# Optimization experiments

Hardware: AMD Instinct MI355X
Metric: run time of the kernel (lower is better)

## Reference

```python
import jax, jax.numpy as jnp
import numpy as np

B, T, IN, H = 64, 512, 128, 512


def _lstm_layer(x, W_ih, W_hh, b_ih, b_hh):
    """Single unidirectional LSTM layer, batch_first input x: [B,T,in].
    PyTorch gate order: i, f, g, o. Returns outputs [B,T,H]."""
    # Precompute input contribution for all timesteps: [T,B,4H]
    xg = jnp.einsum('bti,gi->tbg', x, W_ih) + (b_ih + b_hh)
    Bt = x.shape[0]
    h0 = jnp.zeros((Bt, W_hh.shape[1]), x.dtype)
    c0 = jnp.zeros_like(h0)

    def step(carry, xt):
        h, c = carry
        g = xt + h @ W_hh.T  # [B,4H]
        i, f, gg, o = jnp.split(g, 4, axis=-1)
        i = jax.nn.sigmoid(i)
        f = jax.nn.sigmoid(f)
        gg = jnp.tanh(gg)
        o = jax.nn.sigmoid(o)
        c = f * c + i * gg
        h = o * jnp.tanh(c)
        return (h, c), h

    (_, _), hs = jax.lax.scan(step, (h0, c0), xg)
    return jnp.transpose(hs, (1, 0, 2))  # [B,T,H]


def setup_inputs() -> dict:
    key = jax.random.key(0)
    ks = jax.random.split(key, 11)
    s_in = 1.0 / np.sqrt(H)  # PyTorch LSTM init scale U(-1/sqrt(H), 1/sqrt(H))
    u = lambda k, shape: jax.random.uniform(k, shape, jnp.float32, -s_in, s_in)
    return {
        'x': jax.random.normal(ks[0], (B, T, IN), jnp.float32),
        'W_ih0': u(ks[1], (4 * H, IN)),
        'W_hh0': u(ks[2], (4 * H, H)),
        'b_ih0': u(ks[3], (4 * H,)),
        'b_hh0': u(ks[4], (4 * H,)),
        'W_ih1': u(ks[5], (4 * H, H)),
        'W_hh1': u(ks[6], (4 * H, H)),
        'b_ih1': u(ks[7], (4 * H,)),
        'b_hh1': u(ks[8], (4 * H,)),
        'W_fc': u(ks[9], (1, H)),
        'b_fc': u(ks[10], (1,)),
    }


def reference(x, W_ih0, W_hh0, b_ih0, b_hh0, W_ih1, W_hh1, b_ih1, b_hh1, W_fc, b_fc):
    out = _lstm_layer(x, W_ih0, W_hh0, b_ih0, b_hh0)
    out = _lstm_layer(out, W_ih1, W_hh1, b_ih1, b_hh1)
    logits = out[:, -1, :] @ W_fc.T + b_fc  # [B,1]
    return logits
```

## Files before the change

kernel.cpp:

```cpp
#include <hip/hip_runtime.h>


#define NWG 64
#define NB 64
#define NT 512
#define NH 512
#define FPAD 16

typedef float f32x4 __attribute__((ext_vector_type(4)));
typedef __bf16 bf16x4 __attribute__((ext_vector_type(4)));
typedef __bf16 bf16x8 __attribute__((ext_vector_type(8)));

__device__ __forceinline__ bf16x4 ld8_bypass(const __bf16* p) {
    unsigned long long v = __hip_atomic_load((const unsigned long long*)p,
                                             __ATOMIC_RELAXED, __HIP_MEMORY_SCOPE_AGENT);
    bf16x4 r; __builtin_memcpy(&r, &v, 8); return r;
}

__device__ __forceinline__ void st8_bypass(__bf16* p, unsigned long long v) {
    __hip_atomic_store((unsigned long long*)p, v, __ATOMIC_RELAXED, __HIP_MEMORY_SCOPE_AGENT);
}

__device__ __forceinline__ void wait_flags(const unsigned* flags, unsigned target, int lane) {
    int guard = 0;
    for (;;) {
        unsigned f = __hip_atomic_load((unsigned*)&flags[lane * FPAD],
                                       __ATOMIC_RELAXED, __HIP_MEMORY_SCOPE_AGENT);
        if (__all((int)(f >= target))) break;
        if (++guard > (1 << 17)) break;
    }
}

__global__ void prep_kernel(unsigned short* hs0, unsigned short* hs1, unsigned* flags) {
    int i = blockIdx.x * blockDim.x + threadIdx.x;
    if (i < 2 * NWG * NB * 8) { hs0[i] = 0; hs1[i] = 0; }
    if (i < 2 * NWG * FPAD) flags[i] = 0;
}

template<int KIH, int IS_L0>
__device__ __forceinline__ void layer_body(
    char* Wl, float (*gbuf)[36], float (*c_lds)[8], unsigned short (*hstage)[8],
    int wg,
    const float* __restrict__ W_ih, const float* __restrict__ W_hh,
    const float* __restrict__ b_ih, const float* __restrict__ b_hh,
    const float* __restrict__ x_f32,
    const __bf16* __restrict__ h_in_all,
    __bf16* __restrict__ h_out_all,
    __bf16* __restrict__ hbuf,
    float* __restrict__ h_final,
    unsigned* __restrict__ flags_self,
    const unsigned* __restrict__ flags_dep)
{
    constexpr int KTOT = KIH + NH;
    constexpr int NCH_A = KIH / 32;
    constexpr int NCH_B = NH / 32;
    constexpr int ROWB = KTOT * 2;
    constexpr int BLK = NB * 8;

    const int tid = threadIdx.x;
    const int hcol0 = wg * 8;

    {
        constexpr int CPR = KTOT / 8;
        for (int cid = tid; cid < 32 * CPR; cid += 512) {
            const int r = cid / CPR;
            const int k0 = (cid - r * CPR) * 8;
            const int grow = (r >> 3) * NH + hcol0 + (r & 7);
            const float* src = (k0 < KIH) ? (W_ih + (size_t)grow * KIH + k0)
                                          : (W_hh + (size_t)grow * NH + (k0 - KIH));
            union { __bf16 h[8]; uint4 u; } tmp;
            #pragma unroll
            for (int j = 0; j < 8; ++j) tmp.h[j] = (__bf16)src[j];
            const unsigned off = (unsigned)(r * ROWB) +
                (((unsigned)(2 * k0)) ^ ((unsigned)((r & 7) << 4)));
            *(uint4*)(Wl + off) = tmp.u;
        }
    }

    const int eb = tid >> 3, ec = tid & 7;
    const int hcE = hcol0 + ec;
    const float bI = b_ih[hcE]          + b_hh[hcE];
    const float bF = b_ih[NH + hcE]     + b_hh[NH + hcE];
    const float bG = b_ih[2 * NH + hcE] + b_hh[2 * NH + hcE];
    const float bO = b_ih[3 * NH + hcE] + b_hh[3 * NH + hcE];
    c_lds[eb][ec] = 0.0f;
    __syncthreads();

    const int lane = tid & 63;
    const int wid = tid >> 6;
    const int bt = (wid & 3) * 16;
    const int gt = (wid >> 2) * 16;
    const int arow = bt + (lane & 15);
    const int q4 = ((lane >> 4) & 3) * 4;
    const int brow = gt + (lane & 15);
    const char* wrow = Wl + brow * ROWB;
    const unsigned bsz = (unsigned)((brow & 7) << 4);

    const int aoff = arow * 8 + (q4 & 4);
    const int bsub = (q4 >> 3);

    auto wfrag = [&](int k0) -> bf16x8 {
        const bf16x4 blo = *(const bf16x4*)(wrow + (((unsigned)(2 * (k0 + q4))) ^ bsz));
        const bf16x4 bhi = *(const bf16x4*)(wrow + (((unsigned)(2 * (k0 + 16 + q4))) ^ bsz));
        return __builtin_shufflevector(blo, bhi, 0, 1, 2, 3, 4, 5, 6, 7);
    };

    for (int t = 0; t < NT; ++t) {
        const __bf16* __restrict__ hprev = hbuf + (size_t)(t & 1) * NWG * BLK;
        __bf16* __restrict__ hout = hbuf + (size_t)((t + 1) & 1) * NWG * BLK;

        f32x4 accA0 = {0.f,0.f,0.f,0.f}, accA1 = {0.f,0.f,0.f,0.f};
        f32x4 accB0 = {0.f,0.f,0.f,0.f}, accB1 = {0.f,0.f,0.f,0.f};

        if constexpr (IS_L0 != 0) {
            const float* xb = x_f32 + ((size_t)arow * NT + t) * KIH;
            bf16x8 av[NCH_A];
            #pragma unroll
            for (int kk = 0; kk < NCH_A; ++kk) {
                const float4 lo = *(const float4*)(xb + kk * 32 + q4);
                const float4 hi = *(const float4*)(xb + kk * 32 + 16 + q4);
                const bf16x4 alo = {(__bf16)lo.x, (__bf16)lo.y, (__bf16)lo.z, (__bf16)lo.w};
                const bf16x4 ahi = {(__bf16)hi.x, (__bf16)hi.y, (__bf16)hi.z, (__bf16)hi.w};
                av[kk] = __builtin_shufflevector(alo, ahi, 0, 1, 2, 3, 4, 5, 6, 7);
            }
            #pragma unroll
            for (int kk = 0; kk < NCH_A; ++kk) {
                f32x4& a = (kk & 1) ? accA1 : accA0;
                a = __builtin_amdgcn_mfma_f32_16x16x32_bf16(av[kk], wfrag(kk * 32), a, 0, 0, 0);
            }
            if (t > 0 && wid == 0) wait_flags(flags_self, (unsigned)t, lane);
            __syncthreads();
        } else {
            if (wid == 0) wait_flags(flags_dep, (unsigned)(t + 1), lane);
            if (wid == 1 && t > 0) wait_flags(flags_self, (unsigned)t, lane);
            __syncthreads();
        }

        bf16x4 aBlo[NCH_B], aBhi[NCH_B];
        #pragma unroll
        for (int kk = 0; kk < NCH_B; ++kk) {
            const __bf16* base = hprev + (4 * kk + bsub) * BLK + aoff;
            aBlo[kk] = ld8_bypass(base);
            aBhi[kk] = ld8_bypass(base + 2 * BLK);
        }
        if constexpr (IS_L0 == 0) {
            const __bf16* hA = h_in_all + (size_t)t * NWG * BLK;
            bf16x4 aAlo[NCH_A], aAhi[NCH_A];
            #pragma unroll
            for (int kk = 0; kk < NCH_A; ++kk) {
                const __bf16* base = hA + (4 * kk + bsub) * BLK + aoff;
                aAlo[kk] = ld8_bypass(base);
                aAhi[kk] = ld8_bypass(base + 2 * BLK);
            }
            #pragma unroll
            for (int kk = 0; kk < NCH_A; ++kk) {
                f32x4& a = (kk & 1) ? accA1 : accA0;
                const bf16x8 av = __builtin_shufflevector(aAlo[kk], aAhi[kk], 0,1,2,3,4,5,6,7);
                a = __builtin_amdgcn_mfma_f32_16x16x32_bf16(av, wfrag(kk * 32), a, 0, 0, 0);
            }
        }
        #pragma unroll
        for (int kk = 0; kk < NCH_B; ++kk) {
            f32x4& a = (kk & 1) ? accB1 : accB0;
            const bf16x8 av = __builtin_shufflevector(aBlo[kk], aBhi[kk], 0,1,2,3,4,5,6,7);
            a = __builtin_amdgcn_mfma_f32_16x16x32_bf16(av, wfrag(KIH + kk * 32), a, 0, 0, 0);
        }

        const f32x4 acc = (accA0 + accA1) + (accB0 + accB1);

        #pragma unroll
        for (int i = 0; i < 4; ++i)
            gbuf[bt + ((lane >> 4) & 3) * 4 + i][gt + (lane & 15)] = acc[i];
        __syncthreads();

        {
            const float gi = gbuf[eb][ec]      + bI;
            const float gf = gbuf[eb][8 + ec]  + bF;
            const float gg = gbuf[eb][16 + ec] + bG;
            const float go = gbuf[eb][24 + ec] + bO;
            const float ii = 1.0f / (1.0f + __expf(-gi));
            const float ff = 1.0f / (1.0f + __expf(-gf));
            const float g2 = 2.0f / (1.0f + __expf(-2.0f * gg)) - 1.0f;
            const float oo = 1.0f / (1.0f + __expf(-go));
            const float cn = ff * c_lds[eb][ec] + ii * g2;
            const float th = 2.0f / (1.0f + __expf(-2.0f * cn)) - 1.0f;
            const float hn = oo * th;
            c_lds[eb][ec] = cn;
            const __bf16 hb = (__bf16)hn;
            unsigned short ub;
            __builtin_memcpy(&ub, &hb, 2);
            hstage[eb][ec] = ub;
            if constexpr (IS_L0 == 0) {
                if (t == NT - 1) h_final[(size_t)eb * NH + hcol0 + ec] = hn;
            }
        }
        __syncthreads();

        if (tid < 128) {
            unsigned long long v;
            __builtin_memcpy(&v, &hstage[tid >> 1][(tid & 1) * 4], 8);
            st8_bypass(hout + (size_t)wg * BLK + tid * 4, v);
            if constexpr (IS_L0 != 0)
                st8_bypass(h_out_all + ((size_t)t * NWG + wg) * BLK + tid * 4, v);
        }
        asm volatile("s_waitcnt vmcnt(0)" ::: "memory");
        __syncthreads();
        if (tid == 0)
            __hip_atomic_store(&flags_self[wg * FPAD], (unsigned)(t + 1),
                               __ATOMIC_RELAXED, __HIP_MEMORY_SCOPE_AGENT);
    }
}

__launch_bounds__(512, 2)
__global__ void lstm_fused_kernel(
    const float* W_ih0, const float* W_hh0, const float* b_ih0, const float* b_hh0,
    const float* W_ih1, const float* W_hh1, const float* b_ih1, const float* b_hh1,
    const float* x, __bf16* h0_all, __bf16* hs0, __bf16* hs1,
    float* hfin, unsigned* flags0, unsigned* flags1)
{
    __shared__ __align__(16) char Wl[32 * 2048];
    __shared__ float gbuf[64][36];
    __shared__ float c_lds[64][8];
    __shared__ unsigned short hstage[64][8];

    if (blockIdx.x < NWG) {
        layer_body<128, 1>(Wl, gbuf, c_lds, hstage, blockIdx.x,
                           W_ih0, W_hh0, b_ih0, b_hh0,
                           x, nullptr, h0_all, hs0, nullptr, flags0, nullptr);
    } else {
        layer_body<512, 0>(Wl, gbuf, c_lds, hstage, blockIdx.x - NWG,
                           W_ih1, W_hh1, b_ih1, b_hh1,
                           nullptr, h0_all, nullptr, hs1, hfin, flags1, flags0);
    }
}

__global__ void fc_kernel(const float* __restrict__ hfin,
                          const float* __restrict__ w_fc,
                          const float* __restrict__ b_fc,
                          float* __restrict__ out) {
    __shared__ float red[64][9];
    const int tid = threadIdx.x;
    const int b = tid >> 3, p = tid & 7;
    const int k0 = p * 64;
    float s = 0.f;
    #pragma unroll 8
    for (int k = 0; k < 64; ++k) s += hfin[(size_t)b * NH + k0 + k] * w_fc[k0 + k];
    red[b][p] = s;
    __syncthreads();
    if (p == 0) {
        float a = 0.f;
        #pragma unroll
        for (int j = 0; j < 8; ++j) a += red[b][j];
        out[b] = a + b_fc[0];
    }
}

extern "C" void kernel_launch(void* const* d_in, const int* in_sizes, int n_in,
                              void* d_out, int out_size, void* d_ws, size_t ws_size,
                              hipStream_t stream) {
    const float* x     = (const float*)d_in[0];
    const float* W_ih0 = (const float*)d_in[1];
    const float* W_hh0 = (const float*)d_in[2];
    const float* b_ih0 = (const float*)d_in[3];
    const float* b_hh0 = (const float*)d_in[4];
    const float* W_ih1 = (const float*)d_in[5];
    const float* W_hh1 = (const float*)d_in[6];
    const float* b_ih1 = (const float*)d_in[7];
    const float* b_hh1 = (const float*)d_in[8];
    const float* W_fc  = (const float*)d_in[9];
    const float* b_fc  = (const float*)d_in[10];

    char* ws = (char*)d_ws;
    __bf16*  h0_all = (__bf16*)(ws);
    __bf16*  hs0    = (__bf16*)(ws + 33554432);
    __bf16*  hs1    = (__bf16*)(ws + 33554432 + 131072);
    float*   hfin   = (float*) (ws + 33554432 + 262144);
    unsigned* flags0 = (unsigned*)(ws + 33554432 + 393216);
    unsigned* flags1 = flags0 + NWG * FPAD;

    prep_kernel<<<dim3(256), dim3(256), 0, stream>>>(
        (unsigned short*)hs0, (unsigned short*)hs1, flags0);

    lstm_fused_kernel<<<dim3(2 * NWG), dim3(512), 0, stream>>>(
        W_ih0, W_hh0, b_ih0, b_hh0, W_ih1, W_hh1, b_ih1, b_hh1,
        x, h0_all, hs0, hs1, hfin, flags0, flags1);

    fc_kernel<<<dim3(1), dim3(512), 0, stream>>>(hfin, W_fc, b_fc, (float*)d_out);
}
```

Baseline: 3.117 ms.

## Replace per-workgroup step flags with per-timestep arrival counters and drop ping-pong buffer

The cross-workgroup handshake changes from 64 padded per-workgroup flags to per-timestep counters split into 8 sub-counters. Each workgroup atomically increments one sub-counter, and waiters poll only 8 addresses instead of 64 separate cache lines. Layer 0 now reads its previous hidden state straight from the full h_out_all history, so the duplicate store into a ping-pong buffer is removed. The trade-off is atomic fetch_add contention (8 writers per sub-counter) and counter arrays sized by the number of timesteps.

```diff
diff --git a/kernel.cpp b/kernel.cpp
--- a/kernel.cpp
+++ b/kernel.cpp
@@ -5,7 +5,6 @@
 #define NB 64
 #define NT 512
 #define NH 512
-#define FPAD 16
 
 typedef float f32x4 __attribute__((ext_vector_type(4)));
 typedef __bf16 bf16x4 __attribute__((ext_vector_type(4)));
@@ -21,20 +20,22 @@
     __hip_atomic_store((unsigned long long*)p, v, __ATOMIC_RELAXED, __HIP_MEMORY_SCOPE_AGENT);
 }
 
-__device__ __forceinline__ void wait_flags(const unsigned* flags, unsigned target, int lane) {
+__device__ __forceinline__ void wait_cnt(const unsigned* cnt, int t, int lane) {
+    const unsigned* p = cnt + t * 16 + (lane & 7);
     int guard = 0;
     for (;;) {
-        unsigned f = __hip_atomic_load((unsigned*)&flags[lane * FPAD],
-                                       __ATOMIC_RELAXED, __HIP_MEMORY_SCOPE_AGENT);
-        if (__all((int)(f >= target))) break;
+        unsigned f = __hip_atomic_load((unsigned*)p, __ATOMIC_RELAXED,
+                                       __HIP_MEMORY_SCOPE_AGENT);
+        if (__all((int)(f >= 8u))) break;
         if (++guard > (1 << 17)) break;
     }
 }
 
-__global__ void prep_kernel(unsigned short* hs0, unsigned short* hs1, unsigned* flags) {
+__global__ void prep_kernel(unsigned short* hinit, unsigned short* hs1, unsigned* cnts) {
     int i = blockIdx.x * blockDim.x + threadIdx.x;
-    if (i < 2 * NWG * NB * 8) { hs0[i] = 0; hs1[i] = 0; }
-    if (i < 2 * NWG * FPAD) flags[i] = 0;
+    if (i < NWG * NB * 8) hinit[i] = 0;
+    if (i < 2 * NWG * NB * 8) hs1[i] = 0;
+    if (i < 2 * NT * 16) cnts[i] = 0;
 }
 
 template<int KIH, int IS_L0>
@@ -46,10 +47,11 @@
     const float* __restrict__ x_f32,
     const __bf16* __restrict__ h_in_all,
     __bf16* __restrict__ h_out_all,
+    const __bf16* __restrict__ hinit,
     __bf16* __restrict__ hbuf,
     float* __restrict__ h_final,
-    unsigned* __restrict__ flags_self,
-    const unsigned* __restrict__ flags_dep)
+    unsigned* __restrict__ cnt_self,
+    const unsigned* __restrict__ cnt_dep)
 {
     constexpr int KTOT = KIH + NH;
     constexpr int NCH_A = KIH / 32;
@@ -106,8 +108,15 @@
     };
 
     for (int t = 0; t < NT; ++t) {
-        const __bf16* __restrict__ hprev = hbuf + (size_t)(t & 1) * NWG * BLK;
-        __bf16* __restrict__ hout = hbuf + (size_t)((t + 1) & 1) * NWG * BLK;
+        const __bf16* __restrict__ hprev;
+        __bf16* __restrict__ hout;
+        if constexpr (IS_L0 != 0) {
+            hprev = (t == 0) ? hinit : (h_out_all + (size_t)(t - 1) * NWG * BLK);
+            hout = h_out_all + (size_t)t * NWG * BLK;
+        } else {
+            hprev = hbuf + (size_t)(t & 1) * NWG * BLK;
+            hout = hbuf + (size_t)((t + 1) & 1) * NWG * BLK;
+        }
 
         f32x4 accA0 = {0.f,0.f,0.f,0.f}, accA1 = {0.f,0.f,0.f,0.f};
         f32x4 accB0 = {0.f,0.f,0.f,0.f}, accB1 = {0.f,0.f,0.f,0.f};
@@ -128,11 +137,11 @@
                 f32x4& a = (kk & 1) ? accA1 : accA0;
                 a = __builtin_amdgcn_mfma_f32_16x16x32_bf16(av[kk], wfrag(kk * 32), a, 0, 0, 0);
             }
-            if (t > 0 && wid == 0) wait_flags(flags_self, (unsigned)t, lane);
+            if (t > 0 && wid == 0) wait_cnt(cnt_self, t - 1, lane);
             __syncthreads();
         } else {
-            if (wid == 0) wait_flags(flags_dep, (unsigned)(t + 1), lane);
-            if (wid == 1 && t > 0) wait_flags(flags_self, (unsigned)t, lane);
+            if (wid == 0) wait_cnt(cnt_dep, t, lane);
+            if (wid == 1 && t > 0) wait_cnt(cnt_self, t - 1, lane);
             __syncthreads();
         }
 
@@ -200,14 +209,12 @@
             unsigned long long v;
             __builtin_memcpy(&v, &hstage[tid >> 1][(tid & 1) * 4], 8);
             st8_bypass(hout + (size_t)wg * BLK + tid * 4, v);
-            if constexpr (IS_L0 != 0)
-                st8_bypass(h_out_all + ((size_t)t * NWG + wg) * BLK + tid * 4, v);
         }
         asm volatile("s_waitcnt vmcnt(0)" ::: "memory");
         __syncthreads();
         if (tid == 0)
-            __hip_atomic_store(&flags_self[wg * FPAD], (unsigned)(t + 1),
-                               __ATOMIC_RELAXED, __HIP_MEMORY_SCOPE_AGENT);
+            __hip_atomic_fetch_add(&cnt_self[t * 16 + (wg & 7)], 1u,
+                                   __ATOMIC_RELAXED, __HIP_MEMORY_SCOPE_AGENT);
     }
 }
 
@@ -215,8 +222,8 @@
 __global__ void lstm_fused_kernel(
     const float* W_ih0, const float* W_hh0, const float* b_ih0, const float* b_hh0,
     const float* W_ih1, const float* W_hh1, const float* b_ih1, const float* b_hh1,
-    const float* x, __bf16* h0_all, __bf16* hs0, __bf16* hs1,
-    float* hfin, unsigned* flags0, unsigned* flags1)
+    const float* x, __bf16* h0_all, __bf16* hinit, __bf16* hs1,
+    float* hfin, unsigned* cnt0, unsigned* cnt1)
 {
     __shared__ __align__(16) char Wl[32 * 2048];
     __shared__ float gbuf[64][36];
@@ -226,11 +233,11 @@
     if (blockIdx.x < NWG) {
         layer_body<128, 1>(Wl, gbuf, c_lds, hstage, blockIdx.x,
                            W_ih0, W_hh0, b_ih0, b_hh0,
-                           x, nullptr, h0_all, hs0, nullptr, flags0, nullptr);
+                           x, nullptr, h0_all, hinit, nullptr, nullptr, cnt0, nullptr);
     } else {
         layer_body<512, 0>(Wl, gbuf, c_lds, hstage, blockIdx.x - NWG,
                            W_ih1, W_hh1, b_ih1, b_hh1,
-                           nullptr, h0_all, nullptr, hs1, hfin, flags1, flags0);
+                           nullptr, h0_all, nullptr, nullptr, hs1, hfin, cnt1, cnt0);
     }
 }
 
@@ -272,18 +279,18 @@
 
     char* ws = (char*)d_ws;
     __bf16*  h0_all = (__bf16*)(ws);
-    __bf16*  hs0    = (__bf16*)(ws + 33554432);
-    __bf16*  hs1    = (__bf16*)(ws + 33554432 + 131072);
-    float*   hfin   = (float*) (ws + 33554432 + 262144);
-    unsigned* flags0 = (unsigned*)(ws + 33554432 + 393216);
-    unsigned* flags1 = flags0 + NWG * FPAD;
+    __bf16*  hinit  = (__bf16*)(ws + 33554432);
+    __bf16*  hs1    = (__bf16*)(ws + 33554432 + 65536);
+    float*   hfin   = (float*) (ws + 33554432 + 196608);
+    unsigned* cnt0  = (unsigned*)(ws + 33554432 + 327680);
+    unsigned* cnt1  = cnt0 + NT * 16;
 
     prep_kernel<<<dim3(256), dim3(256), 0, stream>>>(
-        (unsigned short*)hs0, (unsigned short*)hs1, flags0);
+        (unsigned short*)hinit, (unsigned short*)hs1, cnt0);
 
     lstm_fused_kernel<<<dim3(2 * NWG), dim3(512), 0, stream>>>(
         W_ih0, W_hh0, b_ih0, b_hh0, W_ih1, W_hh1, b_ih1, b_hh1,
-        x, h0_all, hs0, hs1, hfin, flags0, flags1);
+        x, h0_all, hinit, hs1, hfin, cnt0, cnt1);
 
     fc_kernel<<<dim3(1), dim3(512), 0, stream>>>(hfin, W_fc, b_fc, (float*)d_out);
 }
```

Result: slower. 3.611 ms (+15.8%).
